# Performance work log

Measured on AMD Instinct MI355X. Metric: run time of the kernel, lower is better.

## Reference

```python
import jax, jax.numpy as jnp
import numpy as np

SCALE = 100.0

def square_distance(src, dst):
    # src: [B,N,D], dst: [B,M,D] -> [B,N,M] squared euclidean distances
    d = -2.0 * jnp.einsum('bnd,bmd->bnm', src, dst)
    d = d + jnp.sum(src * src, axis=-1)[:, :, None]
    d = d + jnp.sum(dst * dst, axis=-1)[:, None, :]
    return d

def setup_inputs() -> dict:
    key = jax.random.key(0)
    k1, k2 = jax.random.split(key)
    B, N, M, D = 8, 8192, 8192, 3
    pred = jax.random.normal(k1, (B, N, D), dtype=jnp.float32)
    gt = jax.random.normal(k2, (B, M, D), dtype=jnp.float32)
    return {"pred": pred, "gt": gt}

def reference(pred, gt):
    dis = square_distance(pred, gt)              # [B,N,M]
    pred_to_gt = jnp.min(dis, axis=2).mean(axis=1)  # [B]
    gt_to_pred = jnp.min(dis, axis=1).mean(axis=1)  # [B]
    return (0.5 * pred_to_gt + 0.5 * gt_to_pred).mean() * SCALE
```

## Files before the change

### kernel.cpp

```cpp
#include <hip/hip_runtime.h>


#define B_DIM 8
#define N_DIM 8192
#define MT    (N_DIM / 32)
#define CH    16
#define NC    (MT / CH)
#define BLOCK 256

typedef short  bf16x8 __attribute__((ext_vector_type(8)));
typedef float  f32x16 __attribute__((ext_vector_type(16)));

__device__ __forceinline__ unsigned short bf16_rne(float f) {
    unsigned int u = __float_as_uint(f);
    u += 0x7fffu + ((u >> 16) & 1u);
    return (unsigned short)(u >> 16);
}
__device__ __forceinline__ float bf16f(unsigned short h) {
    return __uint_as_float(((unsigned int)h) << 16);
}

__global__ __launch_bounds__(256) void chamfer_prep(
    const float* __restrict__ pred, const float* __restrict__ gt,
    unsigned short* __restrict__ bpack)
{
    const int i   = blockIdx.x * 256 + threadIdx.x;
    const int dir = i >> 16;
    const int bm  = i & 0xFFFF;
    const float* dst = dir ? pred : gt;
    const float x = dst[3*bm+0], y = dst[3*bm+1], z = dst[3*bm+2];
    const unsigned short hx = bf16_rne(x), hy = bf16_rne(y), hz = bf16_rne(z);
    const unsigned short lx = bf16_rne(x - bf16f(hx));
    const unsigned short ly = bf16_rne(y - bf16f(hy));
    const unsigned short lz = bf16_rne(z - bf16f(hz));
    const float gn = x*x + y*y + z*z;
    const unsigned short gnh = bf16_rne(gn), gnl = bf16_rne(gn - bf16f(gnh));
    const unsigned short one = 0x3F80;

    const int b  = bm >> 13, m = bm & (N_DIM - 1);
    const int mt = m >> 5,   n = m & 31;
    const int dirb = (dir << 3) | b;
    unsigned short* p0 = bpack + ((size_t)(dirb * MT + mt) * 64 + n) * 8;
    unsigned short* p1 = p0 + 32 * 8;
    bf16x8 h0 = {(short)hx,(short)hy,(short)hz,(short)lx,(short)ly,(short)lz,(short)hx,(short)hy};
    bf16x8 h1 = {(short)hz,(short)one,(short)one,(short)gnh,(short)gnl,0,0,0};
    *(bf16x8*)p0 = h0;
    *(bf16x8*)p1 = h1;
}

__global__ __launch_bounds__(BLOCK, 4) void chamfer_partial(
    const float* __restrict__ pred, const float* __restrict__ gt,
    const bf16x8* __restrict__ bpack, float* __restrict__ minv)
{
    __shared__ bf16x8 sbuf[2][CH * 64];
    const int dirb = blockIdx.x;
    const int dir  = dirb >> 3, b = dirb & 7;
    const int w    = threadIdx.x >> 6, lane = threadIdx.x & 63;
    const int half = lane >> 5,  col = lane & 31;
    const int ntile = blockIdx.y * 4 + w;

    const float* src  = dir ? gt : pred;
    const float* srcb = src + (size_t)b * N_DIM * 3;

    const int n = ntile * 32 + col;
    const float x = srcb[3*n+0], y = srcb[3*n+1], z = srcb[3*n+2];
    const float ax = -2.f*x, ay = -2.f*y, az = -2.f*z;
    const unsigned short ahx = bf16_rne(ax), ahy = bf16_rne(ay), ahz = bf16_rne(az);
    const unsigned short alx = bf16_rne(ax - bf16f(ahx));
    const unsigned short aly = bf16_rne(ay - bf16f(ahy));
    const unsigned short alz = bf16_rne(az - bf16f(ahz));
    const float pn = x*x + y*y + z*z;
    const unsigned short pnh = bf16_rne(pn), pnl = bf16_rne(pn - bf16f(pnh));
    const unsigned short one = 0x3F80;
    bf16x8 a0 = {(short)ahx,(short)ahy,(short)ahz,(short)ahx,(short)ahy,(short)ahz,(short)alx,(short)aly};
    bf16x8 a1 = {(short)alz,(short)pnh,(short)pnl,(short)one,(short)one,0,0,0};
    const bf16x8 afrag = (half == 0) ? a0 : a1;

    const bf16x8* bp = bpack + (size_t)dirb * MT * 64;
    const f32x16 czero = {0.f,0.f,0.f,0.f,0.f,0.f,0.f,0.f,
                          0.f,0.f,0.f,0.f,0.f,0.f,0.f,0.f};
    float best[16];
    #pragma unroll
    for (int r = 0; r < 16; ++r) best[r] = 1e30f;

    bf16x8 rg[4];
    const int soff = w * 256 + lane;
    #define GLOAD(c) { const bf16x8* g = bp + (size_t)(c) * (CH*64) + soff; \
        _Pragma("unroll") for (int i = 0; i < 4; ++i) rg[i] = g[i * 64]; }
    #define SWRITE(pb) { bf16x8* s = &sbuf[pb][soff]; \
        _Pragma("unroll") for (int i = 0; i < 4; ++i) s[i * 64] = rg[i]; }

    GLOAD(0); SWRITE(0); GLOAD(1);
    __syncthreads();

    for (int c = 0; c < NC; ++c) {
        const int pb = c & 1;
        if (c + 1 < NC) SWRITE(pb ^ 1);
        if (c + 2 < NC) GLOAD(c + 2);
        #pragma unroll
        for (int j = 0; j < CH; ++j) {
            const bf16x8 bc = sbuf[pb][j * 64 + lane];
            f32x16 d = __builtin_amdgcn_mfma_f32_32x32x16_bf16(afrag, bc, czero, 0, 0, 0);
            #pragma unroll
            for (int r = 0; r < 16; ++r) best[r] = fminf(best[r], d[r]);
        }
        __syncthreads();
    }

    #pragma unroll
    for (int r = 0; r < 16; ++r) {
        float v = best[r];
        v = fminf(v, __shfl_xor(v, 1,  64));
        v = fminf(v, __shfl_xor(v, 2,  64));
        v = fminf(v, __shfl_xor(v, 4,  64));
        v = fminf(v, __shfl_xor(v, 8,  64));
        v = fminf(v, __shfl_xor(v, 16, 64));
        best[r] = v;
    }
    float* mb = minv + (size_t)dirb * N_DIM + ntile * 32;
    #pragma unroll
    for (int r = 0; r < 16; ++r) {
        const int row = (r & 3) + 8 * (r >> 2) + 4 * half;
        if (col == r) mb[row] = best[r];
    }
}

__global__ __launch_bounds__(256) void chamfer_reduce(
    const float* __restrict__ minv, float* __restrict__ out)
{
    const float scale = 100.0f * 0.5f / ((float)B_DIM * (float)N_DIM);
    const int i = blockIdx.x * 256 + threadIdx.x;
    const float4 v = ((const float4*)minv)[i];
    float s = (v.x + v.y) + (v.z + v.w);
    for (int off = 32; off > 0; off >>= 1) s += __shfl_down(s, off, 64);
    __shared__ float wsum[4];
    if ((threadIdx.x & 63) == 0) wsum[threadIdx.x >> 6] = s;
    __syncthreads();
    if (threadIdx.x == 0)
        atomicAdd(out, (wsum[0] + wsum[1] + wsum[2] + wsum[3]) * scale);
}

extern "C" void kernel_launch(void* const* d_in, const int* in_sizes, int n_in,
                              void* d_out, int out_size, void* d_ws, size_t ws_size,
                              hipStream_t stream) {
    const float* pred = (const float*)d_in[0];
    const float* gt   = (const float*)d_in[1];
    float* out = (float*)d_out;
    unsigned short* bpack = (unsigned short*)d_ws;
    float* minv = (float*)((char*)d_ws + (size_t)16 * MT * 64 * 16);

    hipMemsetAsync(out, 0, sizeof(float), stream);

    chamfer_prep<<<(2 * B_DIM * N_DIM) / 256, 256, 0, stream>>>(pred, gt, bpack);

    dim3 grid(16, N_DIM / (32 * 4));
    chamfer_partial<<<grid, BLOCK, 0, stream>>>(pred, gt, (const bf16x8*)bpack, minv);

    chamfer_reduce<<<(2 * B_DIM * N_DIM) / (256 * 4), 256, 0, stream>>>(minv, out);
}
```

Before: 99.18 us.

## Process two query tiles per wave and fuse final reduction into main kernel

Each wave now handles two 32-point query tiles, reusing every B fragment loaded from shared memory for two MFMAs. This halves LDS reads and the global staging traffic per unit of work. The separate reduce kernel and the memset are removed: the per-block sums are atomically added straight to the output, and the output is zeroed inside the prep kernel. The cost is more registers (launch bounds drop to 2 blocks per CU), half as many blocks, and many more float atomics on a single address.

```diff
diff --git a/kernel.cpp b/kernel.cpp
--- a/kernel.cpp
+++ b/kernel.cpp
@@ -7,6 +7,7 @@
 #define CH    16
 #define NC    (MT / CH)
 #define BLOCK 256
+#define PPW   2
 
 typedef short  bf16x8 __attribute__((ext_vector_type(8)));
 typedef float  f32x16 __attribute__((ext_vector_type(16)));
@@ -22,9 +23,10 @@
 
 __global__ __launch_bounds__(256) void chamfer_prep(
     const float* __restrict__ pred, const float* __restrict__ gt,
-    unsigned short* __restrict__ bpack)
+    unsigned short* __restrict__ bpack, float* __restrict__ out)
 {
     const int i   = blockIdx.x * 256 + threadIdx.x;
+    if (i == 0) out[0] = 0.0f;
     const int dir = i >> 16;
     const int bm  = i & 0xFFFF;
     const float* dst = dir ? pred : gt;
@@ -38,9 +40,9 @@
     const unsigned short one = 0x3F80;
 
     const int b  = bm >> 13, m = bm & (N_DIM - 1);
-    const int mt = m >> 5,   n = m & 31;
+    const int mt = m >> 5,   c = m & 31;
     const int dirb = (dir << 3) | b;
-    unsigned short* p0 = bpack + ((size_t)(dirb * MT + mt) * 64 + n) * 8;
+    unsigned short* p0 = bpack + ((size_t)(dirb * MT + mt) * 64 + c) * 8;
     unsigned short* p1 = p0 + 32 * 8;
     bf16x8 h0 = {(short)hx,(short)hy,(short)hz,(short)lx,(short)ly,(short)lz,(short)hx,(short)hy};
     bf16x8 h1 = {(short)hz,(short)one,(short)one,(short)gnh,(short)gnl,0,0,0};
@@ -48,40 +50,47 @@
     *(bf16x8*)p1 = h1;
 }
 
-__global__ __launch_bounds__(BLOCK, 4) void chamfer_partial(
+__global__ __launch_bounds__(BLOCK, 2) void chamfer_partial(
     const float* __restrict__ pred, const float* __restrict__ gt,
-    const bf16x8* __restrict__ bpack, float* __restrict__ minv)
+    const bf16x8* __restrict__ bpack, float* __restrict__ out)
 {
     __shared__ bf16x8 sbuf[2][CH * 64];
+    __shared__ float wsum[4];
     const int dirb = blockIdx.x;
     const int dir  = dirb >> 3, b = dirb & 7;
     const int w    = threadIdx.x >> 6, lane = threadIdx.x & 63;
     const int half = lane >> 5,  col = lane & 31;
-    const int ntile = blockIdx.y * 4 + w;
 
     const float* src  = dir ? gt : pred;
     const float* srcb = src + (size_t)b * N_DIM * 3;
 
-    const int n = ntile * 32 + col;
-    const float x = srcb[3*n+0], y = srcb[3*n+1], z = srcb[3*n+2];
-    const float ax = -2.f*x, ay = -2.f*y, az = -2.f*z;
-    const unsigned short ahx = bf16_rne(ax), ahy = bf16_rne(ay), ahz = bf16_rne(az);
-    const unsigned short alx = bf16_rne(ax - bf16f(ahx));
-    const unsigned short aly = bf16_rne(ay - bf16f(ahy));
-    const unsigned short alz = bf16_rne(az - bf16f(ahz));
-    const float pn = x*x + y*y + z*z;
-    const unsigned short pnh = bf16_rne(pn), pnl = bf16_rne(pn - bf16f(pnh));
-    const unsigned short one = 0x3F80;
-    bf16x8 a0 = {(short)ahx,(short)ahy,(short)ahz,(short)ahx,(short)ahy,(short)ahz,(short)alx,(short)aly};
-    bf16x8 a1 = {(short)alz,(short)pnh,(short)pnl,(short)one,(short)one,0,0,0};
-    const bf16x8 afrag = (half == 0) ? a0 : a1;
+    bf16x8 afrag[PPW];
+    #pragma unroll
+    for (int p = 0; p < PPW; ++p) {
+        const int ntile = (blockIdx.y * 4 + w) * PPW + p;
+        const int n = ntile * 32 + col;
+        const float x = srcb[3*n+0], y = srcb[3*n+1], z = srcb[3*n+2];
+        const float ax = -2.f*x, ay = -2.f*y, az = -2.f*z;
+        const unsigned short ahx = bf16_rne(ax), ahy = bf16_rne(ay), ahz = bf16_rne(az);
+        const unsigned short alx = bf16_rne(ax - bf16f(ahx));
+        const unsigned short aly = bf16_rne(ay - bf16f(ahy));
+        const unsigned short alz = bf16_rne(az - bf16f(ahz));
+        const float pn = x*x + y*y + z*z;
+        const unsigned short pnh = bf16_rne(pn), pnl = bf16_rne(pn - bf16f(pnh));
+        const unsigned short one = 0x3F80;
+        bf16x8 a0 = {(short)ahx,(short)ahy,(short)ahz,(short)ahx,(short)ahy,(short)ahz,(short)alx,(short)aly};
+        bf16x8 a1 = {(short)alz,(short)pnh,(short)pnl,(short)one,(short)one,0,0,0};
+        afrag[p] = (half == 0) ? a0 : a1;
+    }
 
     const bf16x8* bp = bpack + (size_t)dirb * MT * 64;
     const f32x16 czero = {0.f,0.f,0.f,0.f,0.f,0.f,0.f,0.f,
                           0.f,0.f,0.f,0.f,0.f,0.f,0.f,0.f};
-    float best[16];
+    float best[PPW][16];
     #pragma unroll
-    for (int r = 0; r < 16; ++r) best[r] = 1e30f;
+    for (int p = 0; p < PPW; ++p)
+        #pragma unroll
+        for (int r = 0; r < 16; ++r) best[p][r] = 1e30f;
 
     bf16x8 rg[4];
     const int soff = w * 256 + lane;
@@ -97,47 +106,41 @@
         const int pb = c & 1;
         if (c + 1 < NC) SWRITE(pb ^ 1);
         if (c + 2 < NC) GLOAD(c + 2);
-        #pragma unroll
+        #pragma unroll 8
         for (int j = 0; j < CH; ++j) {
             const bf16x8 bc = sbuf[pb][j * 64 + lane];
-            f32x16 d = __builtin_amdgcn_mfma_f32_32x32x16_bf16(afrag, bc, czero, 0, 0, 0);
             #pragma unroll
-            for (int r = 0; r < 16; ++r) best[r] = fminf(best[r], d[r]);
+            for (int p = 0; p < PPW; ++p) {
+                f32x16 d = __builtin_amdgcn_mfma_f32_32x32x16_bf16(afrag[p], bc, czero, 0, 0, 0);
+                #pragma unroll
+                for (int r = 0; r < 16; ++r) best[p][r] = fminf(best[p][r], d[r]);
+            }
         }
         __syncthreads();
     }
 
+    float bsum = 0.f;
     #pragma unroll
-    for (int r = 0; r < 16; ++r) {
-        float v = best[r];
-        v = fminf(v, __shfl_xor(v, 1,  64));
-        v = fminf(v, __shfl_xor(v, 2,  64));
-        v = fminf(v, __shfl_xor(v, 4,  64));
-        v = fminf(v, __shfl_xor(v, 8,  64));
-        v = fminf(v, __shfl_xor(v, 16, 64));
-        best[r] = v;
+    for (int p = 0; p < PPW; ++p) {
+        float s = 0.f;
+        #pragma unroll
+        for (int r = 0; r < 16; ++r) {
+            float v = best[p][r];
+            v = fminf(v, __shfl_xor(v, 1,  64));
+            v = fminf(v, __shfl_xor(v, 2,  64));
+            v = fminf(v, __shfl_xor(v, 4,  64));
+            v = fminf(v, __shfl_xor(v, 8,  64));
+            v = fminf(v, __shfl_xor(v, 16, 64));
+            s += v;
+        }
+        bsum += s + __shfl_xor(s, 32, 64);
     }
-    float* mb = minv + (size_t)dirb * N_DIM + ntile * 32;
-    #pragma unroll
-    for (int r = 0; r < 16; ++r) {
-        const int row = (r & 3) + 8 * (r >> 2) + 4 * half;
-        if (col == r) mb[row] = best[r];
+    if (lane == 0) wsum[w] = bsum;
+    __syncthreads();
+    if (threadIdx.x == 0) {
+        const float scale = 100.0f * 0.5f / ((float)B_DIM * (float)N_DIM);
+        atomicAdd(out, (wsum[0] + wsum[1] + wsum[2] + wsum[3]) * scale);
     }
-}
-
-__global__ __launch_bounds__(256) void chamfer_reduce(
-    const float* __restrict__ minv, float* __restrict__ out)
-{
-    const float scale = 100.0f * 0.5f / ((float)B_DIM * (float)N_DIM);
-    const int i = blockIdx.x * 256 + threadIdx.x;
-    const float4 v = ((const float4*)minv)[i];
-    float s = (v.x + v.y) + (v.z + v.w);
-    for (int off = 32; off > 0; off >>= 1) s += __shfl_down(s, off, 64);
-    __shared__ float wsum[4];
-    if ((threadIdx.x & 63) == 0) wsum[threadIdx.x >> 6] = s;
-    __syncthreads();
-    if (threadIdx.x == 0)
-        atomicAdd(out, (wsum[0] + wsum[1] + wsum[2] + wsum[3]) * scale);
 }
 
 extern "C" void kernel_launch(void* const* d_in, const int* in_sizes, int n_in,
@@ -147,14 +150,9 @@
     const float* gt   = (const float*)d_in[1];
     float* out = (float*)d_out;
     unsigned short* bpack = (unsigned short*)d_ws;
-    float* minv = (float*)((char*)d_ws + (size_t)16 * MT * 64 * 16);
 
-    hipMemsetAsync(out, 0, sizeof(float), stream);
+    chamfer_prep<<<(2 * B_DIM * N_DIM) / 256, 256, 0, stream>>>(pred, gt, bpack, out);
 
-    chamfer_prep<<<(2 * B_DIM * N_DIM) / 256, 256, 0, stream>>>(pred, gt, bpack);
-
-    dim3 grid(16, N_DIM / (32 * 4));
-    chamfer_partial<<<grid, BLOCK, 0, stream>>>(pred, gt, (const bf16x8*)bpack, minv);
-
-    chamfer_reduce<<<(2 * B_DIM * N_DIM) / (256 * 4), 256, 0, stream>>>(minv, out);
+    dim3 grid(16, N_DIM / (32 * 4 * PPW));
+    chamfer_partial<<<grid, BLOCK, 0, stream>>>(pred, gt, (const bf16x8*)bpack, out);
 }
```

Result: faster. 94.27 us (-5.0%).
